# Optimization experiments

Hardware: AMD Instinct MI355X
Metric: run time of the kernel (lower is better)

## Reference

```python
import jax, jax.numpy as jnp
import numpy as np

N_NODES = 50000
N_EDGES = 800000
D_IN = 96
D_OUT = 96


def setup_inputs() -> dict:
    key = jax.random.key(0)
    k1, k2, k3 = jax.random.split(key, 3)
    x = jax.random.normal(k1, (N_NODES, D_IN), dtype=jnp.float32)
    edge_index = jax.random.randint(k2, (2, N_EDGES), 0, N_NODES, dtype=jnp.int64)
    edge_weight = jnp.ones((N_EDGES,), dtype=jnp.float32)
    # Glorot-ish init for the linear weight, zero bias (as in PyG GCNConv)
    W = jax.random.normal(k3, (D_IN, D_OUT), dtype=jnp.float32) * (1.0 / np.sqrt(D_IN))
    b = jnp.zeros((D_OUT,), dtype=jnp.float32)
    return {"x": x, "edge_index": edge_index, "edge_weight": edge_weight, "W": W, "b": b}


def reference(x, edge_index, edge_weight, W, b):
    """PyG GCNConv: out = D^{-1/2} (A + I) D^{-1/2} (x @ W) + b."""
    N = x.shape[0]
    row, col = edge_index[0], edge_index[1]  # source -> target
    # add self loops with weight 1 (PyG default add_self_loops=True)
    loop = jnp.arange(N, dtype=edge_index.dtype)
    row = jnp.concatenate([row, loop])
    col = jnp.concatenate([col, loop])
    ew = jnp.concatenate([edge_weight, jnp.ones((N,), dtype=edge_weight.dtype)])
    # symmetric normalization based on (weighted) in-degree over col
    deg = jax.ops.segment_sum(ew, col, num_segments=N)  # [N]
    dinv = jnp.where(deg > 0, jax.lax.rsqrt(deg), 0.0)
    norm = dinv[row] * ew * dinv[col]  # [E+N]
    # linear transform first (small GEMM), then gather-scale-scatter over edges
    h = x @ W  # [N, D_OUT]
    msg = h[row] * norm[:, None]  # [E+N, D_OUT]
    out = jax.ops.segment_sum(msg, col, num_segments=N)  # [N, D_OUT]
    return out + b
```

## Files before the change

kernel.cpp:

```cpp
#include <hip/hip_runtime.h>

#define N_NODES 50000
#define N_EDGES 800000
#define D 96
#define NBKT 256
#define BNODES 196
#define BCAP 4608
#define PART_B 500
#define EPB (N_EDGES / PART_B)
#define CAP 48
#define GCAP 1536

__device__ __forceinline__ float bf_lo(unsigned u) { return __uint_as_float(u << 16); }
__device__ __forceinline__ float bf_hi(unsigned u) { return __uint_as_float(u & 0xFFFF0000u); }
__device__ __forceinline__ unsigned f2bf_bits(unsigned u) {
    return (u + 0x7FFFu + ((u >> 16) & 1u)) & 0xFFFF0000u;
}

__global__ __launch_bounds__(256) void k_zero(int* __restrict__ bkt_cnt) {
    bkt_cnt[threadIdx.x] = 0;
}

__global__ __launch_bounds__(256) void k_part(const int* __restrict__ row,
                                              const int* __restrict__ col,
                                              const float* __restrict__ ew,
                                              int* __restrict__ bkt_cnt,
                                              uint2* __restrict__ bktbuf) {
    __shared__ int hist[NBKT];
    __shared__ int cur[NBKT];
    int tid = threadIdx.x;
    hist[tid] = 0;
    __syncthreads();
    int e0 = blockIdx.x * EPB;
    for (int i = tid; i < EPB; i += 256)
        atomicAdd(&hist[col[e0 + i] / BNODES], 1);
    __syncthreads();
    cur[tid] = atomicAdd(&bkt_cnt[tid], hist[tid]);
    __syncthreads();
    for (int i = tid; i < EPB; i += 256) {
        int e = e0 + i;
        int c = col[e];
        int b = c / BNODES;
        int p = atomicAdd(&cur[b], 1);
        if (p < BCAP)
            bktbuf[(size_t)b * BCAP + p] =
                make_uint2((unsigned)row[e] | ((unsigned)(c - b * BNODES) << 16),
                           __float_as_uint(ew[e]));
    }
}

__global__ __launch_bounds__(256) void k_bin(const int* __restrict__ bkt_cnt,
                                             const uint2* __restrict__ bktbuf,
                                             unsigned* __restrict__ recs,
                                             int* __restrict__ rowptr,
                                             float* __restrict__ deg) {
    __shared__ int sbkt[NBKT];
    __shared__ int lcnt[BNODES];
    __shared__ int loff[256];
    __shared__ unsigned lslot[BNODES * CAP];
    int tid = threadIdx.x;
    int b = blockIdx.x;

    sbkt[tid] = min(bkt_cnt[tid], BCAP);
    __syncthreads();
    for (int off = 1; off < 256; off <<= 1) {
        int t = (tid >= off) ? sbkt[tid - off] : 0;
        __syncthreads();
        sbkt[tid] += t;
        __syncthreads();
    }
    int ne = min(bkt_cnt[b], BCAP);
    int gbase = sbkt[b] - ne;

    for (int i = tid; i < BNODES; i += 256) lcnt[i] = 0;
    __syncthreads();

    for (int i = tid; i < ne; i += 256) {
        uint2 r = bktbuf[(size_t)b * BCAP + i];
        int lc = (int)(r.x >> 16);
        int p = atomicAdd(&lcnt[lc], 1);
        if (p < CAP) lslot[lc * CAP + p] = f2bf_bits(r.y) | (r.x & 0xFFFFu);
    }
    __syncthreads();

    int myv = (tid < BNODES) ? min(lcnt[tid], CAP) : 0;
    loff[tid] = myv;
    __syncthreads();
    for (int off = 1; off < 256; off <<= 1) {
        int t = (tid >= off) ? loff[tid - off] : 0;
        __syncthreads();
        loff[tid] += t;
        __syncthreads();
    }
    int excl = loff[tid] - myv;
    __syncthreads();
    loff[tid] = excl;
    __syncthreads();

    for (int i = tid; i < BNODES * CAP; i += 256) {
        int ln = i / CAP, s = i % CAP;
        if (s < min(lcnt[ln], CAP))
            recs[gbase + loff[ln] + s] = lslot[i];
    }
    int base = b * BNODES;
    for (int i = tid; i < BNODES; i += 256) {
        int n = base + i;
        if (n <= N_NODES) rowptr[n] = gbase + loff[i];
        if (n < N_NODES) {
            int cn = min(lcnt[i], CAP);
            float d = 1.0f;
            for (int k = 0; k < cn; ++k) d += bf_hi(lslot[i * CAP + k]);
            deg[n] = d;
        }
    }
}

__global__ __launch_bounds__(256) void k_gemm(const float* __restrict__ x,
                                              const float* __restrict__ W,
                                              const float* __restrict__ deg,
                                              unsigned short* __restrict__ hb) {
    __shared__ float Wl[D * D];
    int tid = threadIdx.x;
    const float4* Wg4 = (const float4*)W;
    float4* Wl4 = (float4*)Wl;
    for (int i = tid; i < D * D / 4; i += 256) Wl4[i] = Wg4[i];
    __syncthreads();

    int jg = tid % 24;
    int ng = tid / 24;
    bool active = (ng < 10);
    int j = jg * 4;
    int node0 = blockIdx.x * 40 + ng * 4;

    float acc[4][4] = {};
    if (active) {
        for (int k4 = 0; k4 < D / 4; ++k4) {
            float4 xv[4];
#pragma unroll
            for (int i = 0; i < 4; ++i)
                xv[i] = *(const float4*)&x[(node0 + i) * D + k4 * 4];
#pragma unroll
            for (int kk = 0; kk < 4; ++kk) {
                float4 w4 = *(const float4*)&Wl[(k4 * 4 + kk) * D + j];
#pragma unroll
                for (int i = 0; i < 4; ++i) {
                    float xs = (kk == 0) ? xv[i].x : (kk == 1) ? xv[i].y
                             : (kk == 2) ? xv[i].z : xv[i].w;
                    acc[i][0] += xs * w4.x;
                    acc[i][1] += xs * w4.y;
                    acc[i][2] += xs * w4.z;
                    acc[i][3] += xs * w4.w;
                }
            }
        }
#pragma unroll
        for (int i = 0; i < 4; ++i) {
            int n = node0 + i;
            float dg = deg[n];
            float di = dg > 0.0f ? rsqrtf(dg) : 0.0f;
            ushort4 pk;
            pk.x = (unsigned short)(f2bf_bits(__float_as_uint(acc[i][0] * di)) >> 16);
            pk.y = (unsigned short)(f2bf_bits(__float_as_uint(acc[i][1] * di)) >> 16);
            pk.z = (unsigned short)(f2bf_bits(__float_as_uint(acc[i][2] * di)) >> 16);
            pk.w = (unsigned short)(f2bf_bits(__float_as_uint(acc[i][3] * di)) >> 16);
            *(ushort4*)&hb[(size_t)n * D + j] = pk;
        }
    }
}

__global__ __launch_bounds__(192) void k_gather(const int* __restrict__ rowptr,
                                                const unsigned* __restrict__ recs,
                                                const unsigned short* __restrict__ hb,
                                                const float* __restrict__ deg,
                                                const float* __restrict__ bias,
                                                float* __restrict__ out) {
    __shared__ unsigned sre[GCAP];
    __shared__ int sptr[17];
    int tid = threadIdx.x;
    int nb = blockIdx.x * 16;

    if (tid < 17) sptr[tid] = rowptr[nb + tid];
    __syncthreads();
    int e0 = sptr[0];
    int stage = min(sptr[16] - e0, GCAP);
    for (int i = tid; i < stage; i += 192) sre[i] = recs[e0 + i];
    __syncthreads();

    int local = tid / 12;
    int jq = tid % 12;
    int n = nb + local;
    int j = jq * 8;

    uint4 sv = *(const uint4*)(hb + (size_t)n * D + j);
    float acc[8];
    acc[0] = bf_lo(sv.x); acc[1] = bf_hi(sv.x);
    acc[2] = bf_lo(sv.y); acc[3] = bf_hi(sv.y);
    acc[4] = bf_lo(sv.z); acc[5] = bf_hi(sv.z);
    acc[6] = bf_lo(sv.w); acc[7] = bf_hi(sv.w);

    int ls = sptr[local] - e0;
    int le = sptr[local + 1] - e0;
    for (int idx = ls; idx < le; ++idx) {
        unsigned rec = (idx < GCAP) ? sre[idx] : recs[e0 + idx];
        float w = bf_hi(rec);
        int src = (int)(rec & 0xFFFFu);
        uint4 v = *(const uint4*)(hb + (size_t)src * D + j);
        acc[0] += w * bf_lo(v.x); acc[1] += w * bf_hi(v.x);
        acc[2] += w * bf_lo(v.y); acc[3] += w * bf_hi(v.y);
        acc[4] += w * bf_lo(v.z); acc[5] += w * bf_hi(v.z);
        acc[6] += w * bf_lo(v.w); acc[7] += w * bf_hi(v.w);
    }

    float dg = deg[n];
    float di = dg > 0.0f ? rsqrtf(dg) : 0.0f;
    float4 b0 = *(const float4*)&bias[j];
    float4 b1 = *(const float4*)&bias[j + 4];
    float4 o0, o1;
    o0.x = acc[0] * di + b0.x; o0.y = acc[1] * di + b0.y;
    o0.z = acc[2] * di + b0.z; o0.w = acc[3] * di + b0.w;
    o1.x = acc[4] * di + b1.x; o1.y = acc[5] * di + b1.y;
    o1.z = acc[6] * di + b1.z; o1.w = acc[7] * di + b1.w;
    *(float4*)&out[(size_t)n * D + j] = o0;
    *(float4*)&out[(size_t)n * D + j + 4] = o1;
}

extern "C" void kernel_launch(void* const* d_in, const int* in_sizes, int n_in,
                              void* d_out, int out_size, void* d_ws, size_t ws_size,
                              hipStream_t stream) {
    const float* x  = (const float*)d_in[0];
    const int*   ei = (const int*)d_in[1];
    const float* ew = (const float*)d_in[2];
    const float* W  = (const float*)d_in[3];
    const float* b  = (const float*)d_in[4];
    float* out = (float*)d_out;

    const int* row = ei;
    const int* col = ei + N_EDGES;

    char* p = (char*)d_ws;
    unsigned short* hb     = (unsigned short*)p;
    uint2*          bktbuf = (uint2*)p;            p += (size_t)N_NODES * D * 2;
    unsigned*       recs   = (unsigned*)p;         p += (size_t)N_EDGES * 4;
    int*            rowptr = (int*)p;              p += (size_t)(N_NODES + 16) * 4;
    float*          deg    = (float*)p;            p += (size_t)N_NODES * 4;
    int*            bkt_cnt= (int*)p;              p += (size_t)NBKT * 4;

    k_zero  <<<1, 256, 0, stream>>>(bkt_cnt);
    k_part  <<<PART_B, 256, 0, stream>>>(row, col, ew, bkt_cnt, bktbuf);
    k_bin   <<<NBKT, 256, 0, stream>>>(bkt_cnt, bktbuf, recs, rowptr, deg);
    k_gemm  <<<1250, 256, 0, stream>>>(x, W, deg, hb);
    k_gather<<<(N_NODES + 15) / 16, 192, 0, stream>>>(rowptr, recs, hb, deg, b, out);
}
```

Measured before the change: 160.3 us.

## Use wave-shuffle scans, precompute dinv, unroll gather, nontemporal stores, halve partition blocks

Several small changes at once. The LDS-based block scans in the binning kernel become wave shuffle scans, and rsqrt of the degree is computed once in binning rather than in both downstream kernels. The gather loop is unrolled by two so more row loads are in flight, and output stores become nontemporal. The zero kernel is replaced by hipMemsetAsync, and the partition grid is halved, which gives each block more edges but lowers parallelism.

Measured after the change: 152.8 us. -4.7%, faster.

```diff
diff --git a/kernel.cpp b/kernel.cpp
--- a/kernel.cpp
+++ b/kernel.cpp
@@ -6,10 +6,12 @@
 #define NBKT 256
 #define BNODES 196
 #define BCAP 4608
-#define PART_B 500
+#define PART_B 250
 #define EPB (N_EDGES / PART_B)
 #define CAP 48
 #define GCAP 1536
+
+typedef float vfloat4 __attribute__((ext_vector_type(4)));
 
 __device__ __forceinline__ float bf_lo(unsigned u) { return __uint_as_float(u << 16); }
 __device__ __forceinline__ float bf_hi(unsigned u) { return __uint_as_float(u & 0xFFFF0000u); }
@@ -17,8 +19,21 @@
     return (u + 0x7FFFu + ((u >> 16) & 1u)) & 0xFFFF0000u;
 }
 
-__global__ __launch_bounds__(256) void k_zero(int* __restrict__ bkt_cnt) {
-    bkt_cnt[threadIdx.x] = 0;
+__device__ __forceinline__ int exscan256(int v, int* wsum) {
+    int lane = threadIdx.x & 63;
+    int wave = threadIdx.x >> 6;
+    int incl = v;
+#pragma unroll
+    for (int off = 1; off < 64; off <<= 1) {
+        int t = __shfl_up(incl, off);
+        if (lane >= off) incl += t;
+    }
+    if (lane == 63) wsum[wave] = incl;
+    __syncthreads();
+    int base = 0;
+#pragma unroll
+    for (int wv = 0; wv < 3; ++wv) base += (wv < wave) ? wsum[wv] : 0;
+    return base + incl - v;
 }
 
 __global__ __launch_bounds__(256) void k_part(const int* __restrict__ row,
@@ -53,7 +68,9 @@
                                              const uint2* __restrict__ bktbuf,
                                              unsigned* __restrict__ recs,
                                              int* __restrict__ rowptr,
-                                             float* __restrict__ deg) {
+                                             float* __restrict__ dinv) {
+    __shared__ int wsum1[4];
+    __shared__ int wsum2[4];
     __shared__ int sbkt[NBKT];
     __shared__ int lcnt[BNODES];
     __shared__ int loff[256];
@@ -61,19 +78,13 @@
     int tid = threadIdx.x;
     int b = blockIdx.x;
 
-    sbkt[tid] = min(bkt_cnt[tid], BCAP);
-    __syncthreads();
-    for (int off = 1; off < 256; off <<= 1) {
-        int t = (tid >= off) ? sbkt[tid - off] : 0;
-        __syncthreads();
-        sbkt[tid] += t;
-        __syncthreads();
-    }
+    int bv = min(bkt_cnt[tid], BCAP);
+    int bex = exscan256(bv, wsum1);
+    sbkt[tid] = bex;
+    for (int i = tid; i < BNODES; i += 256) lcnt[i] = 0;
+    __syncthreads();
+    int gbase = sbkt[b];
     int ne = min(bkt_cnt[b], BCAP);
-    int gbase = sbkt[b] - ne;
-
-    for (int i = tid; i < BNODES; i += 256) lcnt[i] = 0;
-    __syncthreads();
 
     for (int i = tid; i < ne; i += 256) {
         uint2 r = bktbuf[(size_t)b * BCAP + i];
@@ -84,17 +95,8 @@
     __syncthreads();
 
     int myv = (tid < BNODES) ? min(lcnt[tid], CAP) : 0;
-    loff[tid] = myv;
-    __syncthreads();
-    for (int off = 1; off < 256; off <<= 1) {
-        int t = (tid >= off) ? loff[tid - off] : 0;
-        __syncthreads();
-        loff[tid] += t;
-        __syncthreads();
-    }
-    int excl = loff[tid] - myv;
-    __syncthreads();
-    loff[tid] = excl;
+    int ex2 = exscan256(myv, wsum2);
+    loff[tid] = ex2;
     __syncthreads();
 
     for (int i = tid; i < BNODES * CAP; i += 256) {
@@ -110,14 +112,14 @@
             int cn = min(lcnt[i], CAP);
             float d = 1.0f;
             for (int k = 0; k < cn; ++k) d += bf_hi(lslot[i * CAP + k]);
-            deg[n] = d;
+            dinv[n] = rsqrtf(d);
         }
     }
 }
 
 __global__ __launch_bounds__(256) void k_gemm(const float* __restrict__ x,
                                               const float* __restrict__ W,
-                                              const float* __restrict__ deg,
+                                              const float* __restrict__ dinv,
                                               unsigned short* __restrict__ hb) {
     __shared__ float Wl[D * D];
     int tid = threadIdx.x;
@@ -156,8 +158,7 @@
 #pragma unroll
         for (int i = 0; i < 4; ++i) {
             int n = node0 + i;
-            float dg = deg[n];
-            float di = dg > 0.0f ? rsqrtf(dg) : 0.0f;
+            float di = dinv[n];
             ushort4 pk;
             pk.x = (unsigned short)(f2bf_bits(__float_as_uint(acc[i][0] * di)) >> 16);
             pk.y = (unsigned short)(f2bf_bits(__float_as_uint(acc[i][1] * di)) >> 16);
@@ -171,7 +172,7 @@
 __global__ __launch_bounds__(192) void k_gather(const int* __restrict__ rowptr,
                                                 const unsigned* __restrict__ recs,
                                                 const unsigned short* __restrict__ hb,
-                                                const float* __restrict__ deg,
+                                                const float* __restrict__ dinv,
                                                 const float* __restrict__ bias,
                                                 float* __restrict__ out) {
     __shared__ unsigned sre[GCAP];
@@ -200,28 +201,42 @@
 
     int ls = sptr[local] - e0;
     int le = sptr[local + 1] - e0;
-    for (int idx = ls; idx < le; ++idx) {
-        unsigned rec = (idx < GCAP) ? sre[idx] : recs[e0 + idx];
-        float w = bf_hi(rec);
-        int src = (int)(rec & 0xFFFFu);
-        uint4 v = *(const uint4*)(hb + (size_t)src * D + j);
-        acc[0] += w * bf_lo(v.x); acc[1] += w * bf_hi(v.x);
-        acc[2] += w * bf_lo(v.y); acc[3] += w * bf_hi(v.y);
-        acc[4] += w * bf_lo(v.z); acc[5] += w * bf_hi(v.z);
-        acc[6] += w * bf_lo(v.w); acc[7] += w * bf_hi(v.w);
-    }
-
-    float dg = deg[n];
-    float di = dg > 0.0f ? rsqrtf(dg) : 0.0f;
+    int idx = ls;
+    for (; idx + 2 <= le; idx += 2) {
+        unsigned r0 = (idx < GCAP) ? sre[idx] : recs[e0 + idx];
+        unsigned r1 = (idx + 1 < GCAP) ? sre[idx + 1] : recs[e0 + idx + 1];
+        uint4 v0 = *(const uint4*)(hb + (size_t)(r0 & 0xFFFFu) * D + j);
+        uint4 v1 = *(const uint4*)(hb + (size_t)(r1 & 0xFFFFu) * D + j);
+        float w0 = bf_hi(r0), w1 = bf_hi(r1);
+        acc[0] += w0 * bf_lo(v0.x); acc[1] += w0 * bf_hi(v0.x);
+        acc[2] += w0 * bf_lo(v0.y); acc[3] += w0 * bf_hi(v0.y);
+        acc[4] += w0 * bf_lo(v0.z); acc[5] += w0 * bf_hi(v0.z);
+        acc[6] += w0 * bf_lo(v0.w); acc[7] += w0 * bf_hi(v0.w);
+        acc[0] += w1 * bf_lo(v1.x); acc[1] += w1 * bf_hi(v1.x);
+        acc[2] += w1 * bf_lo(v1.y); acc[3] += w1 * bf_hi(v1.y);
+        acc[4] += w1 * bf_lo(v1.z); acc[5] += w1 * bf_hi(v1.z);
+        acc[6] += w1 * bf_lo(v1.w); acc[7] += w1 * bf_hi(v1.w);
+    }
+    if (idx < le) {
+        unsigned r0 = (idx < GCAP) ? sre[idx] : recs[e0 + idx];
+        uint4 v0 = *(const uint4*)(hb + (size_t)(r0 & 0xFFFFu) * D + j);
+        float w0 = bf_hi(r0);
+        acc[0] += w0 * bf_lo(v0.x); acc[1] += w0 * bf_hi(v0.x);
+        acc[2] += w0 * bf_lo(v0.y); acc[3] += w0 * bf_hi(v0.y);
+        acc[4] += w0 * bf_lo(v0.z); acc[5] += w0 * bf_hi(v0.z);
+        acc[6] += w0 * bf_lo(v0.w); acc[7] += w0 * bf_hi(v0.w);
+    }
+
+    float di = dinv[n];
     float4 b0 = *(const float4*)&bias[j];
     float4 b1 = *(const float4*)&bias[j + 4];
-    float4 o0, o1;
+    vfloat4 o0, o1;
     o0.x = acc[0] * di + b0.x; o0.y = acc[1] * di + b0.y;
     o0.z = acc[2] * di + b0.z; o0.w = acc[3] * di + b0.w;
     o1.x = acc[4] * di + b1.x; o1.y = acc[5] * di + b1.y;
     o1.z = acc[6] * di + b1.z; o1.w = acc[7] * di + b1.w;
-    *(float4*)&out[(size_t)n * D + j] = o0;
-    *(float4*)&out[(size_t)n * D + j + 4] = o1;
+    __builtin_nontemporal_store(o0, (vfloat4*)&out[(size_t)n * D + j]);
+    __builtin_nontemporal_store(o1, (vfloat4*)&out[(size_t)n * D + j + 4]);
 }
 
 extern "C" void kernel_launch(void* const* d_in, const int* in_sizes, int n_in,
@@ -242,12 +257,12 @@
     uint2*          bktbuf = (uint2*)p;            p += (size_t)N_NODES * D * 2;
     unsigned*       recs   = (unsigned*)p;         p += (size_t)N_EDGES * 4;
     int*            rowptr = (int*)p;              p += (size_t)(N_NODES + 16) * 4;
-    float*          deg    = (float*)p;            p += (size_t)N_NODES * 4;
+    float*          dinv   = (float*)p;            p += (size_t)N_NODES * 4;
     int*            bkt_cnt= (int*)p;              p += (size_t)NBKT * 4;
 
-    k_zero  <<<1, 256, 0, stream>>>(bkt_cnt);
+    (void)hipMemsetAsync(bkt_cnt, 0, NBKT * sizeof(int), stream);
     k_part  <<<PART_B, 256, 0, stream>>>(row, col, ew, bkt_cnt, bktbuf);
-    k_bin   <<<NBKT, 256, 0, stream>>>(bkt_cnt, bktbuf, recs, rowptr, deg);
-    k_gemm  <<<1250, 256, 0, stream>>>(x, W, deg, hb);
-    k_gather<<<(N_NODES + 15) / 16, 192, 0, stream>>>(rowptr, recs, hb, deg, b, out);
-}
+    k_bin   <<<NBKT, 256, 0, stream>>>(bkt_cnt, bktbuf, recs, rowptr, dinv);
+    k_gemm  <<<1250, 256, 0, stream>>>(x, W, dinv, hb);
+    k_gather<<<(N_NODES + 15) / 16, 192, 0, stream>>>(rowptr, recs, hb, dinv, b, out);
+}
```
